# Performance work log

Measured on AMD Instinct MI355X. Metric: run time of the kernel, lower is better.

Reference implementation:

```python
import jax, jax.numpy as jnp
import numpy as np

NUM_HEADS = 16  # matches init_kwargs num_heads
ROPE_BASE = 10000.0


def _rope(x):
    # x: [B, H, T, d_k]; canonical interleaved rotary embedding
    d = x.shape[-1]
    T = x.shape[-2]
    inv_freq = 1.0 / (ROPE_BASE ** (jnp.arange(0, d, 2, dtype=jnp.float32) / d))  # [d/2]
    ang = jnp.arange(T, dtype=jnp.float32)[:, None] * inv_freq[None, :]  # [T, d/2]
    cos, sin = jnp.cos(ang), jnp.sin(ang)  # broadcast over B,H
    x1 = x[..., 0::2]
    x2 = x[..., 1::2]
    even = x1 * cos - x2 * sin
    odd = x1 * sin + x2 * cos
    return jnp.stack([even, odd], axis=-1).reshape(x.shape)


def setup_inputs() -> dict:
    key = jax.random.key(0)
    ks = jax.random.split(key, 5)
    B, T, D = 2, 2048, 2048
    s = 1.0 / np.sqrt(D)
    return {
        "x": jax.random.normal(ks[0], (B, T, D), dtype=jnp.float32),
        "Wkqv": jax.random.normal(ks[1], (D, 3 * D), dtype=jnp.float32) * s,
        "bkqv": jax.random.normal(ks[2], (3 * D,), dtype=jnp.float32) * 0.01,
        "Wo": jax.random.normal(ks[3], (D, D), dtype=jnp.float32) * s,
        "bo": jax.random.normal(ks[4], (D,), dtype=jnp.float32) * 0.01,
    }


def reference(x, Wkqv, bkqv, Wo, bo):
    B, T, D = x.shape
    H = NUM_HEADS
    d_k = D // H
    kqv = x @ Wkqv + bkqv  # [B, T, 3D]
    # split order per source: index 0 = K, 1 = Q, 2 = V
    k, q, v = jnp.split(kqv, 3, axis=-1)

    def heads(t):  # [B, T, D] -> [B, H, T, d_k]
        return t.reshape(B, T, H, d_k).transpose(0, 2, 1, 3)

    k, q, v = heads(k), heads(q), heads(v)
    k = _rope(k)
    q = _rope(q)
    scores = jnp.einsum('bhtd,bhTd->bhtT', q, k)  # [B, H, T, T]
    causal = jnp.triu(jnp.ones((T, T), dtype=bool), k=1)
    scores = jnp.where(causal, -jnp.inf, scores)
    attn = jax.nn.softmax(scores / jnp.sqrt(jnp.float32(d_k)), axis=-1)
    out = jnp.einsum('bhtT,bhTd->bhtd', attn, v)  # [B, H, T, d_k]
    out = out.transpose(0, 2, 1, 3).reshape(B, T, D)
    return out @ Wo + bo
```

## Files before the change

kernel.cpp:

```cpp
#include <hip/hip_runtime.h>
#include <cstdint>
#include <cstddef>

typedef __attribute__((ext_vector_type(4))) float  floatx4;
typedef __attribute__((ext_vector_type(8))) __bf16 bf16x8;
typedef __attribute__((ext_vector_type(4))) __bf16 bf16x4;

#define B_   2
#define T_   2048
#define D_   2048
#define H_   16
#define DK   128
#define BT_  (B_ * T_)
#define N3   (3 * D_)

__device__ __forceinline__ void async_copy16(const void* g, void* l) {
    __builtin_amdgcn_global_load_lds((const __attribute__((address_space(1))) void*)g,
                                     (__attribute__((address_space(3))) void*)l,
                                     16, 0, 0);
}

__global__ void cast_bf16_kernel(const float* __restrict__ in, __bf16* __restrict__ out, int n4) {
    int i = blockIdx.x * 256 + threadIdx.x;
    if (i >= n4) return;
    float4 v = ((const float4*)in)[i];
    bf16x4 o;
    o.x = (__bf16)v.x; o.y = (__bf16)v.y; o.z = (__bf16)v.z; o.w = (__bf16)v.w;
    ((bf16x4*)out)[i] = o;
}

__global__ void transcast_kernel(const float* __restrict__ in, __bf16* __restrict__ out, int R, int C) {
    __shared__ float tile[32][33];
    int c0 = blockIdx.x * 32, r0 = blockIdx.y * 32;
    int tx = threadIdx.x, ty = threadIdx.y;
#pragma unroll
    for (int j = 0; j < 32; j += 8)
        tile[ty + j][tx] = in[(size_t)(r0 + ty + j) * C + c0 + tx];
    __syncthreads();
#pragma unroll
    for (int j = 0; j < 32; j += 8)
        out[(size_t)(c0 + ty + j) * R + r0 + tx] = (__bf16)tile[tx][ty + j];
}

template <typename OutT>
__global__ __launch_bounds__(256)
void gemm_bt(const __bf16* __restrict__ A, const __bf16* __restrict__ BTm,
             const float* __restrict__ bias, OutT* __restrict__ C,
             int M, int N, int K) {
    __shared__ __align__(16) __bf16 As[128 * 64];
    __shared__ __align__(16) __bf16 Bs[128 * 64];
    const int tid  = threadIdx.x;
    const int lane = tid & 63;
    const int wave = tid >> 6;
    const int quad = lane >> 4;
    const int l16  = lane & 15;
    const int m0 = blockIdx.y * 128;
    const int n0 = blockIdx.x * 128;
    const int wm = (wave & 1) * 64;
    const int wn = (wave >> 1) * 64;

    const floatx4 z4 = {0.f, 0.f, 0.f, 0.f};
    floatx4 acc[4][4];
#pragma unroll
    for (int i = 0; i < 4; ++i)
#pragma unroll
        for (int j = 0; j < 4; ++j) acc[i][j] = z4;

    int           sOff[4];
    const __bf16* gA[4];
    const __bf16* gB[4];
#pragma unroll
    for (int i = 0; i < 4; ++i) {
        int s = i * 256 + tid;
        int row = s >> 3, cs = s & 7;
        int gc = cs ^ (row & 7);
        sOff[i] = s * 8;
        gA[i] = A   + (size_t)(m0 + row) * K + gc * 8;
        gB[i] = BTm + (size_t)(n0 + row) * K + gc * 8;
    }

    for (int kt = 0; kt < K; kt += 64) {
        __syncthreads();
#pragma unroll
        for (int i = 0; i < 4; ++i) {
            async_copy16(gA[i] + kt, As + sOff[i]);
            async_copy16(gB[i] + kt, Bs + sOff[i]);
        }
        __syncthreads();
#pragma unroll
        for (int ks2 = 0; ks2 < 2; ++ks2) {
            bf16x8 af[4], bf[4];
#pragma unroll
            for (int t = 0; t < 4; ++t) {
                int rowA = wm + t * 16 + l16;
                int ca = (ks2 * 4 + quad) ^ (rowA & 7);
                af[t] = *(const bf16x8*)(As + rowA * 64 + ca * 8);
                int rowB = wn + t * 16 + l16;
                int cb = (ks2 * 4 + quad) ^ (rowB & 7);
                bf[t] = *(const bf16x8*)(Bs + rowB * 64 + cb * 8);
            }
#pragma unroll
            for (int mt = 0; mt < 4; ++mt)
#pragma unroll
                for (int nt = 0; nt < 4; ++nt)
                    acc[mt][nt] = __builtin_amdgcn_mfma_f32_16x16x32_bf16(af[mt], bf[nt], acc[mt][nt], 0, 0, 0);
        }
    }

#pragma unroll
    for (int nt = 0; nt < 4; ++nt) {
        int n = n0 + wn + nt * 16 + l16;
        float bv = bias[n];
#pragma unroll
        for (int mt = 0; mt < 4; ++mt)
#pragma unroll
            for (int r = 0; r < 4; ++r) {
                int m = m0 + wm + mt * 16 + quad * 4 + r;
                C[(size_t)m * N + n] = (OutT)(acc[mt][nt][r] + bv);
            }
    }
}

__global__ __launch_bounds__(256)
void gemm_kqv(const __bf16* __restrict__ A, const __bf16* __restrict__ BTm,
              const float* __restrict__ bias,
              __bf16* __restrict__ Kh, __bf16* __restrict__ Qh,
              __bf16* __restrict__ VT,
              int M, int N, int K) {
    __shared__ __align__(16) __bf16 As[128 * 64];
    __shared__ __align__(16) __bf16 Bs[128 * 64];
    const int tid  = threadIdx.x;
    const int lane = tid & 63;
    const int wave = tid >> 6;
    const int quad = lane >> 4;
    const int l16  = lane & 15;
    const int m0 = blockIdx.y * 128;
    const int n0 = blockIdx.x * 128;
    const int wm = (wave & 1) * 64;
    const int wn = (wave >> 1) * 64;

    const floatx4 z4 = {0.f, 0.f, 0.f, 0.f};
    floatx4 acc[4][4];
#pragma unroll
    for (int i = 0; i < 4; ++i)
#pragma unroll
        for (int j = 0; j < 4; ++j) acc[i][j] = z4;

    int           sOff[4];
    const __bf16* gA[4];
    const __bf16* gB[4];
#pragma unroll
    for (int i = 0; i < 4; ++i) {
        int s = i * 256 + tid;
        int row = s >> 3, cs = s & 7;
        int gc = cs ^ (row & 7);
        sOff[i] = s * 8;
        gA[i] = A   + (size_t)(m0 + row) * K + gc * 8;
        gB[i] = BTm + (size_t)(n0 + row) * K + gc * 8;
    }

    for (int kt = 0; kt < K; kt += 64) {
        __syncthreads();
#pragma unroll
        for (int i = 0; i < 4; ++i) {
            async_copy16(gA[i] + kt, As + sOff[i]);
            async_copy16(gB[i] + kt, Bs + sOff[i]);
        }
        __syncthreads();
#pragma unroll
        for (int ks2 = 0; ks2 < 2; ++ks2) {
            bf16x8 af[4], bf[4];
#pragma unroll
            for (int t = 0; t < 4; ++t) {
                int rowA = wm + t * 16 + l16;
                int ca = (ks2 * 4 + quad) ^ (rowA & 7);
                af[t] = *(const bf16x8*)(As + rowA * 64 + ca * 8);
                int rowB = wn + t * 16 + l16;
                int cb = (ks2 * 4 + quad) ^ (rowB & 7);
                bf[t] = *(const bf16x8*)(Bs + rowB * 64 + cb * 8);
            }
#pragma unroll
            for (int mt = 0; mt < 4; ++mt)
#pragma unroll
                for (int nt = 0; nt < 4; ++nt)
                    acc[mt][nt] = __builtin_amdgcn_mfma_f32_16x16x32_bf16(af[mt], bf[nt], acc[mt][nt], 0, 0, 0);
        }
    }

#pragma unroll
    for (int nt = 0; nt < 4; ++nt) {
        const int n   = n0 + wn + nt * 16 + l16;
        const float bv = bias[n];
        const int which = n >> 11;
        const int nin   = n & (D_ - 1);
        const int h  = nin >> 7;
        const int dd = nin & 127;
        const float freq_rev = 0.15915494309189535f *
                               exp2f((float)(dd >> 1) * (-13.287712379549449f / 64.f));
        const float qscale = (which == 1) ? 0.12751740f : 1.0f;
#pragma unroll
        for (int mt = 0; mt < 4; ++mt)
#pragma unroll
            for (int r = 0; r < 4; ++r) {
                const int m = m0 + wm + mt * 16 + quad * 4 + r;
                const int b = m >> 11;
                const int t = m & (T_ - 1);
                const int bh = b * H_ + h;
                const float val = acc[mt][nt][r] + bv;
                if (which == 2) {
                    VT[((size_t)bh * DK + dd) * T_ + t] = (__bf16)val;
                } else {
                    const float other = __shfl_xor(val, 1);
                    const float x1 = (dd & 1) ? other : val;
                    const float x2 = (dd & 1) ? val : other;
                    float rev = (float)t * freq_rev;
                    rev -= floorf(rev);
                    const float ang = rev * 6.283185307179586f;
                    const float sn = __sinf(ang), cn = __cosf(ang);
                    const float res = (dd & 1) ? (x1 * sn + x2 * cn)
                                               : (x1 * cn - x2 * sn);
                    __bf16* dst = (which == 1) ? Qh : Kh;
                    dst[((size_t)bh * T_ + t) * DK + dd] = (__bf16)(res * qscale);
                }
            }
    }
}

__global__ __launch_bounds__(256)
void fa_kernel(const __bf16* __restrict__ Qg, const __bf16* __restrict__ Kg,
               const __bf16* __restrict__ VTg, __bf16* __restrict__ Og) {
    __shared__ __align__(16) __bf16 Ks[2][64 * 128];
    __shared__ __align__(16) __bf16 Vs[2][128 * 64];
    __shared__ __align__(16) __bf16 Ps[4][16 * 64];
    const int tid  = threadIdx.x;
    const int lane = tid & 63, wave = tid >> 6;
    const int quad = lane >> 4, l16 = lane & 15;
    const int bh = blockIdx.y;
    const int j  = blockIdx.x;
    const int b = bh >> 4, h = bh & 15;

    const __bf16* Kb = Kg  + (size_t)bh * T_ * DK;
    const __bf16* Vb = VTg + (size_t)bh * DK * T_;
    __bf16* Psw = Ps[wave];

    const floatx4 z4 = {0.f, 0.f, 0.f, 0.f};

    int           sK[4], sV[4];
    const __bf16* gK[4];
    const __bf16* gV[4];
#pragma unroll
    for (int i = 0; i < 4; ++i) {
        int s = i * 256 + tid;
        { int row = s >> 4, cs = s & 15; int gc = cs ^ (row & 7);
          sK[i] = s * 8; gK[i] = Kb + (size_t)row * DK + gc * 8; }
        { int row = s >> 3, cs = s & 7;  int gc = cs ^ (row & 7);
          sV[i] = s * 8; gV[i] = Vb + (size_t)row * T_ + gc * 8; }
    }

    for (int half = 0; half < 2; ++half) {
        const int qt = half ? (31 - j) : j;
        const int q0 = qt * 64;

        __syncthreads();
        {
            const __bf16* Qb = Qg + (size_t)(bh * T_ + q0) * DK;
#pragma unroll
            for (int i = 0; i < 4; ++i) {
                int s = i * 256 + tid;
                int row = s >> 4, cs = s & 15;
                int gc = cs ^ (row & 7);
                async_copy16(Qb + row * DK + gc * 8, &Ks[0][0] + s * 8);
            }
        }
        __syncthreads();
        bf16x8 qf[4];
#pragma unroll
        for (int ks = 0; ks < 4; ++ks) {
            int row = wave * 16 + l16;
            int c = (ks * 4 + quad) ^ (row & 7);
            qf[ks] = *(const bf16x8*)(&Ks[0][0] + row * DK + c * 8);
        }
        __syncthreads();

#pragma unroll
        for (int i = 0; i < 4; ++i) async_copy16(gK[i], &Ks[0][0] + sK[i]);
#pragma unroll
        for (int i = 0; i < 4; ++i) async_copy16(gV[i], &Vs[0][0] + sV[i]);

        float m_i[4], l_i[4];
        floatx4 accO[8];
#pragma unroll
        for (int r = 0; r < 4; ++r) { m_i[r] = -1e30f; l_i[r] = 0.f; }
#pragma unroll
        for (int nt = 0; nt < 8; ++nt) accO[nt] = z4;

        for (int kt = 0; kt <= qt; ++kt) {
            const int cur = kt & 1;
            if (kt < qt) {
                const int nb = cur ^ 1;
                const size_t koff = (size_t)(kt + 1) * 64 * DK;
                const size_t voff = (size_t)(kt + 1) * 64;
#pragma unroll
                for (int i = 0; i < 4; ++i) async_copy16(gK[i] + koff, &Ks[nb][0] + sK[i]);
#pragma unroll
                for (int i = 0; i < 4; ++i) async_copy16(gV[i] + voff, &Vs[nb][0] + sV[i]);
                asm volatile("s_waitcnt vmcnt(8)" ::: "memory");
            } else {
                asm volatile("s_waitcnt vmcnt(0)" ::: "memory");
            }
            __builtin_amdgcn_s_barrier();

            const __bf16* Kcur = &Ks[cur][0];
            const __bf16* Vcur = &Vs[cur][0];

            floatx4 sc[4];
#pragma unroll
            for (int nt = 0; nt < 4; ++nt) sc[nt] = z4;
            __builtin_amdgcn_s_setprio(1);
#pragma unroll
            for (int ks = 0; ks < 4; ++ks)
#pragma unroll
                for (int nt = 0; nt < 4; ++nt) {
                    int row = nt * 16 + l16;
                    int c = (ks * 4 + quad) ^ (row & 7);
                    bf16x8 kf = *(const bf16x8*)(Kcur + row * DK + c * 8);
                    sc[nt] = __builtin_amdgcn_mfma_f32_16x16x32_bf16(qf[ks], kf, sc[nt], 0, 0, 0);
                }
            __builtin_amdgcn_s_setprio(0);

            float mnew[4] = {-1e30f, -1e30f, -1e30f, -1e30f};
            if (kt == qt) {
                const int qrow0 = q0 + wave * 16 + quad * 4;
#pragma unroll
                for (int nt = 0; nt < 4; ++nt) {
                    int kp = kt * 64 + nt * 16 + l16;
#pragma unroll
                    for (int r = 0; r < 4; ++r) {
                        float v = sc[nt][r];
                        v = (kp > qrow0 + r) ? -1e30f : v;
                        sc[nt][r] = v;
                        mnew[r] = fmaxf(mnew[r], v);
                    }
                }
            } else {
#pragma unroll
                for (int nt = 0; nt < 4; ++nt)
#pragma unroll
                    for (int r = 0; r < 4; ++r) mnew[r] = fmaxf(mnew[r], sc[nt][r]);
            }
#pragma unroll
            for (int r = 0; r < 4; ++r) {
                float v = mnew[r];
                v = fmaxf(v, __shfl_xor(v, 1));
                v = fmaxf(v, __shfl_xor(v, 2));
                v = fmaxf(v, __shfl_xor(v, 4));
                v = fmaxf(v, __shfl_xor(v, 8));
                mnew[r] = v;
            }
            float alpha[4];
#pragma unroll
            for (int r = 0; r < 4; ++r) {
                float mi = fmaxf(m_i[r], mnew[r]);
                alpha[r] = exp2f(m_i[r] - mi);
                m_i[r] = mi;
            }
            float rs[4] = {0.f, 0.f, 0.f, 0.f};
#pragma unroll
            for (int nt = 0; nt < 4; ++nt)
#pragma unroll
                for (int r = 0; r < 4; ++r) {
                    float p = exp2f(sc[nt][r] - m_i[r]);
                    sc[nt][r] = p;
                    rs[r] += p;
                }
#pragma unroll
            for (int r = 0; r < 4; ++r) {
                float v = rs[r];
                v += __shfl_xor(v, 1);
                v += __shfl_xor(v, 2);
                v += __shfl_xor(v, 4);
                v += __shfl_xor(v, 8);
                l_i[r] = l_i[r] * alpha[r] + v;
            }
#pragma unroll
            for (int nt = 0; nt < 8; ++nt)
#pragma unroll
                for (int r = 0; r < 4; ++r) accO[nt][r] *= alpha[r];

#pragma unroll
            for (int nt = 0; nt < 4; ++nt) {
                int col = nt * 16 + l16;
                int ch = col >> 3, off = col & 7;
#pragma unroll
                for (int r = 0; r < 4; ++r) {
                    int row = quad * 4 + r;
                    Psw[row * 64 + (ch ^ (row & 7)) * 8 + off] = (__bf16)sc[nt][r];
                }
            }
            __builtin_amdgcn_s_setprio(1);
#pragma unroll
            for (int ks2 = 0; ks2 < 2; ++ks2) {
                int ach = (ks2 * 4 + quad) ^ (l16 & 7);
                bf16x8 pf = *(const bf16x8*)(Psw + l16 * 64 + ach * 8);
#pragma unroll
                for (int nt = 0; nt < 8; ++nt) {
                    int vrow = nt * 16 + l16;
                    int vch = (ks2 * 4 + quad) ^ (vrow & 7);
                    bf16x8 vf = *(const bf16x8*)(Vcur + vrow * 64 + vch * 8);
                    accO[nt] = __builtin_amdgcn_mfma_f32_16x16x32_bf16(pf, vf, accO[nt], 0, 0, 0);
                }
            }
            __builtin_amdgcn_s_setprio(0);

            __builtin_amdgcn_s_barrier();
        }

#pragma unroll
        for (int nt = 0; nt < 8; ++nt)
#pragma unroll
            for (int r = 0; r < 4; ++r) {
                int trow = q0 + wave * 16 + quad * 4 + r;
                int col = h * DK + nt * 16 + l16;
                Og[(size_t)(b * T_ + trow) * D_ + col] = (__bf16)(accO[nt][r] / l_i[r]);
            }
    }
}

extern "C" void kernel_launch(void* const* d_in, const int* in_sizes, int n_in,
                              void* d_out, int out_size, void* d_ws, size_t ws_size,
                              hipStream_t stream) {
    const float* x    = (const float*)d_in[0];
    const float* Wkqv = (const float*)d_in[1];
    const float* bkqv = (const float*)d_in[2];
    const float* Wo   = (const float*)d_in[3];
    const float* bo   = (const float*)d_in[4];
    float* out = (float*)d_out;

    char* p = (char*)d_ws;
    __bf16* xb    = (__bf16*)p; p += (size_t)BT_ * D_ * 2;
    __bf16* WkqvT = (__bf16*)p; p += (size_t)D_ * N3 * 2;
    __bf16* WoT   = (__bf16*)p; p += (size_t)D_ * D_ * 2;
    __bf16* qh    = (__bf16*)p; p += (size_t)BT_ * D_ * 2;
    __bf16* kh    = (__bf16*)p; p += (size_t)BT_ * D_ * 2;
    __bf16* vT    = (__bf16*)p; p += (size_t)BT_ * D_ * 2;
    __bf16* ao    = (__bf16*)p; p += (size_t)BT_ * D_ * 2;

    cast_bf16_kernel<<<(BT_ * D_ / 4 + 255) / 256, 256, 0, stream>>>(x, xb, BT_ * D_ / 4);
    transcast_kernel<<<dim3(N3 / 32, D_ / 32), dim3(32, 8), 0, stream>>>(Wkqv, WkqvT, D_, N3);
    transcast_kernel<<<dim3(D_ / 32, D_ / 32), dim3(32, 8), 0, stream>>>(Wo, WoT, D_, D_);
    gemm_kqv<<<dim3(N3 / 128, BT_ / 128), 256, 0, stream>>>(xb, WkqvT, bkqv, kh, qh, vT, BT_, N3, D_);
    fa_kernel<<<dim3(16, B_ * H_), 256, 0, stream>>>(qh, kh, vT, ao);
    gemm_bt<float><<<dim3(D_ / 128, BT_ / 128), 256, 0, stream>>>(ao, WoT, bo, out, BT_, D_, D_);
}
```

Before: 435.3 us.

## Transpose attention MFMA operands and stage V-transpose stores through LDS

The flash-attention kernel swaps the MFMA operand order so each lane owns one query row. The row max and sum reductions then need two cross-lane shuffles instead of many, P is written to LDS as packed 4-element vectors, and the output is stored as contiguous bf16x4 per row. In the KQV GEMM, the V-transpose epilogue is staged through a padded shared-memory tile so VT is written with coalesced 16-byte stores instead of strided scalar stores. The cost is a larger shared buffer in the GEMM plus extra barriers on the V blocks.

Measured after the change: 397.3 us. 1.1x faster.

```diff
diff --git a/kernel.cpp b/kernel.cpp
--- a/kernel.cpp
+++ b/kernel.cpp
@@ -127,8 +127,9 @@
               __bf16* __restrict__ Kh, __bf16* __restrict__ Qh,
               __bf16* __restrict__ VT,
               int M, int N, int K) {
-    __shared__ __align__(16) __bf16 As[128 * 64];
-    __shared__ __align__(16) __bf16 Bs[128 * 64];
+    __shared__ __align__(16) __bf16 smem[128 * 136];
+    __bf16* As = smem;
+    __bf16* Bs = smem + 128 * 64;
     const int tid  = threadIdx.x;
     const int lane = tid & 63;
     const int wave = tid >> 6;
@@ -187,29 +188,51 @@
         }
     }
 
-#pragma unroll
-    for (int nt = 0; nt < 4; ++nt) {
-        const int n   = n0 + wn + nt * 16 + l16;
-        const float bv = bias[n];
-        const int which = n >> 11;
-        const int nin   = n & (D_ - 1);
-        const int h  = nin >> 7;
-        const int dd = nin & 127;
-        const float freq_rev = 0.15915494309189535f *
-                               exp2f((float)(dd >> 1) * (-13.287712379549449f / 64.f));
-        const float qscale = (which == 1) ? 0.12751740f : 1.0f;
-#pragma unroll
-        for (int mt = 0; mt < 4; ++mt)
-#pragma unroll
-            for (int r = 0; r < 4; ++r) {
-                const int m = m0 + wm + mt * 16 + quad * 4 + r;
-                const int b = m >> 11;
-                const int t = m & (T_ - 1);
-                const int bh = b * H_ + h;
-                const float val = acc[mt][nt][r] + bv;
-                if (which == 2) {
-                    VT[((size_t)bh * DK + dd) * T_ + t] = (__bf16)val;
-                } else {
+    const int which = n0 >> 11;
+    const int h  = (n0 & (D_ - 1)) >> 7;
+    const int b  = m0 >> 11;
+    const int t0 = m0 & (T_ - 1);
+    const int bh = b * H_ + h;
+
+    if (which == 2) {
+        __syncthreads();
+#pragma unroll
+        for (int nt = 0; nt < 4; ++nt) {
+            const int n  = n0 + wn + nt * 16 + l16;
+            const float bv = bias[n];
+            const int dd = wn + nt * 16 + l16;
+#pragma unroll
+            for (int mt = 0; mt < 4; ++mt)
+#pragma unroll
+                for (int r = 0; r < 4; ++r) {
+                    const int tl = wm + mt * 16 + quad * 4 + r;
+                    smem[dd * 136 + tl] = (__bf16)(acc[mt][nt][r] + bv);
+                }
+        }
+        __syncthreads();
+#pragma unroll
+        for (int i = 0; i < 8; ++i) {
+            int s = i * 256 + tid;
+            int dd = s >> 4, c = s & 15;
+            bf16x8 vv = *(const bf16x8*)(smem + dd * 136 + c * 8);
+            *(bf16x8*)(VT + ((size_t)bh * DK + dd) * T_ + t0 + c * 8) = vv;
+        }
+    } else {
+        const float qscale = which ? 0.12751740f : 1.0f;
+        __bf16* dst = which ? Qh : Kh;
+#pragma unroll
+        for (int nt = 0; nt < 4; ++nt) {
+            const int n  = n0 + wn + nt * 16 + l16;
+            const float bv = bias[n];
+            const int dd = wn + nt * 16 + l16;
+            const float freq_rev = 0.15915494309189535f *
+                exp2f((float)(dd >> 1) * (-13.287712379549449f / 64.f));
+#pragma unroll
+            for (int mt = 0; mt < 4; ++mt)
+#pragma unroll
+                for (int r = 0; r < 4; ++r) {
+                    const int t = t0 + wm + mt * 16 + quad * 4 + r;
+                    const float val = acc[mt][nt][r] + bv;
                     const float other = __shfl_xor(val, 1);
                     const float x1 = (dd & 1) ? other : val;
                     const float x2 = (dd & 1) ? val : other;
@@ -219,10 +242,9 @@
                     const float sn = __sinf(ang), cn = __cosf(ang);
                     const float res = (dd & 1) ? (x1 * sn + x2 * cn)
                                                : (x1 * cn - x2 * sn);
-                    __bf16* dst = (which == 1) ? Qh : Kh;
                     dst[((size_t)bh * T_ + t) * DK + dd] = (__bf16)(res * qscale);
                 }
-            }
+        }
     }
 }
 
@@ -242,6 +264,7 @@
     const __bf16* Kb = Kg  + (size_t)bh * T_ * DK;
     const __bf16* Vb = VTg + (size_t)bh * DK * T_;
     __bf16* Psw = Ps[wave];
+    const int swzP = (l16 & 7) << 1;
 
     const floatx4 z4 = {0.f, 0.f, 0.f, 0.f};
 
@@ -260,6 +283,7 @@
     for (int half = 0; half < 2; ++half) {
         const int qt = half ? (31 - j) : j;
         const int q0 = qt * 64;
+        const int qpos = q0 + wave * 16 + l16;
 
         __syncthreads();
         {
@@ -287,12 +311,10 @@
 #pragma unroll
         for (int i = 0; i < 4; ++i) async_copy16(gV[i], &Vs[0][0] + sV[i]);
 
-        float m_i[4], l_i[4];
+        float m_i = -1e30f, l_i = 0.f;
         floatx4 accO[8];
 #pragma unroll
-        for (int r = 0; r < 4; ++r) { m_i[r] = -1e30f; l_i[r] = 0.f; }
-#pragma unroll
-        for (int nt = 0; nt < 8; ++nt) accO[nt] = z4;
+        for (int dt = 0; dt < 8; ++dt) accO[dt] = z4;
 
         for (int kt = 0; kt <= qt; ++kt) {
             const int cur = kt & 1;
@@ -324,90 +346,71 @@
                     int row = nt * 16 + l16;
                     int c = (ks * 4 + quad) ^ (row & 7);
                     bf16x8 kf = *(const bf16x8*)(Kcur + row * DK + c * 8);
-                    sc[nt] = __builtin_amdgcn_mfma_f32_16x16x32_bf16(qf[ks], kf, sc[nt], 0, 0, 0);
+                    sc[nt] = __builtin_amdgcn_mfma_f32_16x16x32_bf16(kf, qf[ks], sc[nt], 0, 0, 0);
                 }
             __builtin_amdgcn_s_setprio(0);
 
-            float mnew[4] = {-1e30f, -1e30f, -1e30f, -1e30f};
+            float mnew = -1e30f;
             if (kt == qt) {
-                const int qrow0 = q0 + wave * 16 + quad * 4;
 #pragma unroll
                 for (int nt = 0; nt < 4; ++nt) {
-                    int kp = kt * 64 + nt * 16 + l16;
+                    int kbase = kt * 64 + nt * 16 + quad * 4;
 #pragma unroll
                     for (int r = 0; r < 4; ++r) {
                         float v = sc[nt][r];
-                        v = (kp > qrow0 + r) ? -1e30f : v;
+                        v = (kbase + r > qpos) ? -1e30f : v;
                         sc[nt][r] = v;
-                        mnew[r] = fmaxf(mnew[r], v);
+                        mnew = fmaxf(mnew, v);
                     }
                 }
             } else {
 #pragma unroll
                 for (int nt = 0; nt < 4; ++nt)
 #pragma unroll
-                    for (int r = 0; r < 4; ++r) mnew[r] = fmaxf(mnew[r], sc[nt][r]);
-            }
-#pragma unroll
-            for (int r = 0; r < 4; ++r) {
-                float v = mnew[r];
-                v = fmaxf(v, __shfl_xor(v, 1));
-                v = fmaxf(v, __shfl_xor(v, 2));
-                v = fmaxf(v, __shfl_xor(v, 4));
-                v = fmaxf(v, __shfl_xor(v, 8));
-                mnew[r] = v;
-            }
-            float alpha[4];
-#pragma unroll
-            for (int r = 0; r < 4; ++r) {
-                float mi = fmaxf(m_i[r], mnew[r]);
-                alpha[r] = exp2f(m_i[r] - mi);
-                m_i[r] = mi;
-            }
-            float rs[4] = {0.f, 0.f, 0.f, 0.f};
+                    for (int r = 0; r < 4; ++r) mnew = fmaxf(mnew, sc[nt][r]);
+            }
+            mnew = fmaxf(mnew, __shfl_xor(mnew, 16));
+            mnew = fmaxf(mnew, __shfl_xor(mnew, 32));
+            const float mi = fmaxf(m_i, mnew);
+            const float alpha = exp2f(m_i - mi);
+            m_i = mi;
+
+            float rs = 0.f;
 #pragma unroll
             for (int nt = 0; nt < 4; ++nt)
 #pragma unroll
                 for (int r = 0; r < 4; ++r) {
-                    float p = exp2f(sc[nt][r] - m_i[r]);
-                    sc[nt][r] = p;
-                    rs[r] += p;
-                }
-#pragma unroll
-            for (int r = 0; r < 4; ++r) {
-                float v = rs[r];
-                v += __shfl_xor(v, 1);
-                v += __shfl_xor(v, 2);
-                v += __shfl_xor(v, 4);
-                v += __shfl_xor(v, 8);
-                l_i[r] = l_i[r] * alpha[r] + v;
-            }
-#pragma unroll
-            for (int nt = 0; nt < 8; ++nt)
-#pragma unroll
-                for (int r = 0; r < 4; ++r) accO[nt][r] *= alpha[r];
+                    float pv = exp2f(sc[nt][r] - mi);
+                    sc[nt][r] = pv;
+                    rs += pv;
+                }
+            rs += __shfl_xor(rs, 16);
+            rs += __shfl_xor(rs, 32);
+            l_i = l_i * alpha + rs;
+#pragma unroll
+            for (int dt = 0; dt < 8; ++dt)
+#pragma unroll
+                for (int r = 0; r < 4; ++r) accO[dt][r] *= alpha;
 
 #pragma unroll
             for (int nt = 0; nt < 4; ++nt) {
-                int col = nt * 16 + l16;
-                int ch = col >> 3, off = col & 7;
-#pragma unroll
-                for (int r = 0; r < 4; ++r) {
-                    int row = quad * 4 + r;
-                    Psw[row * 64 + (ch ^ (row & 7)) * 8 + off] = (__bf16)sc[nt][r];
-                }
+                bf16x4 pw;
+                pw.x = (__bf16)sc[nt][0]; pw.y = (__bf16)sc[nt][1];
+                pw.z = (__bf16)sc[nt][2]; pw.w = (__bf16)sc[nt][3];
+                int g = (nt * 4 + quad) ^ swzP;
+                *(bf16x4*)(Psw + l16 * 64 + g * 4) = pw;
             }
             __builtin_amdgcn_s_setprio(1);
 #pragma unroll
-            for (int ks2 = 0; ks2 < 2; ++ks2) {
-                int ach = (ks2 * 4 + quad) ^ (l16 & 7);
-                bf16x8 pf = *(const bf16x8*)(Psw + l16 * 64 + ach * 8);
-#pragma unroll
-                for (int nt = 0; nt < 8; ++nt) {
-                    int vrow = nt * 16 + l16;
-                    int vch = (ks2 * 4 + quad) ^ (vrow & 7);
+            for (int kc = 0; kc < 2; ++kc) {
+                int gk = (kc * 8 + quad * 2) ^ swzP;
+                bf16x8 pb = *(const bf16x8*)(Psw + l16 * 64 + gk * 4);
+#pragma unroll
+                for (int dt = 0; dt < 8; ++dt) {
+                    int vrow = dt * 16 + l16;
+                    int vch = (kc * 4 + quad) ^ (vrow & 7);
                     bf16x8 vf = *(const bf16x8*)(Vcur + vrow * 64 + vch * 8);
-                    accO[nt] = __builtin_amdgcn_mfma_f32_16x16x32_bf16(pf, vf, accO[nt], 0, 0, 0);
+                    accO[dt] = __builtin_amdgcn_mfma_f32_16x16x32_bf16(vf, pb, accO[dt], 0, 0, 0);
                 }
             }
             __builtin_amdgcn_s_setprio(0);
@@ -415,14 +418,17 @@
             __builtin_amdgcn_s_barrier();
         }
 
-#pragma unroll
-        for (int nt = 0; nt < 8; ++nt)
-#pragma unroll
-            for (int r = 0; r < 4; ++r) {
-                int trow = q0 + wave * 16 + quad * 4 + r;
-                int col = h * DK + nt * 16 + l16;
-                Og[(size_t)(b * T_ + trow) * D_ + col] = (__bf16)(accO[nt][r] / l_i[r]);
-            }
+        const float inv = 1.0f / l_i;
+        __bf16* orow = Og + (size_t)(b * T_ + qpos) * D_ + h * DK;
+#pragma unroll
+        for (int dt = 0; dt < 8; ++dt) {
+            bf16x4 ow;
+            ow.x = (__bf16)(accO[dt][0] * inv);
+            ow.y = (__bf16)(accO[dt][1] * inv);
+            ow.z = (__bf16)(accO[dt][2] * inv);
+            ow.w = (__bf16)(accO[dt][3] * inv);
+            *(bf16x4*)(orow + dt * 16 + quad * 4) = ow;
+        }
     }
 }
 
```
